# Kernel optimization log

Hardware: AMD Instinct MI355X
Metric: run time of the kernel (lower is better)

The kernel has to match this reference:

```python
import jax, jax.numpy as jnp
import numpy as np

N, F_IN, H, HEADS, C, E = 4096, 768, 512, 4, 32, 131072
DH = H // HEADS


def gcn_conv(x, W, b, src, dst):
    # PyG GCNConv: add self-loops, symmetric normalization, scatter-add aggregation
    h = x @ W                                   # [N, H_out]
    loop = jnp.arange(N)
    s = jnp.concatenate([src, loop])            # sources incl self-loops
    d = jnp.concatenate([dst, loop])            # targets incl self-loops
    deg = jax.ops.segment_sum(jnp.ones_like(d, dtype=h.dtype), d, num_segments=N)
    dinv = jnp.where(deg > 0, jax.lax.rsqrt(deg), 0.0)
    norm = dinv[s] * dinv[d]                    # [E+N]
    msg = h[s] * norm[:, None]                  # gather + scale
    out = jax.ops.segment_sum(msg, d, num_segments=N)  # scatter-add
    return out + b


def mha(x, in_w, in_b, out_w, out_b):
    # torch.nn.MultiheadAttention, batch=1, q=k=v=x, eval (no dropout)
    qkv = x @ in_w.T + in_b                     # [N, 3H]
    q, k, v = jnp.split(qkv, 3, axis=-1)
    q = q.reshape(N, HEADS, DH)
    k = k.reshape(N, HEADS, DH)
    v = v.reshape(N, HEADS, DH)
    scale = 1.0 / jnp.sqrt(jnp.asarray(DH, x.dtype))
    scores = jnp.einsum('nhd,mhd->hnm', q * scale, k)   # [HEADS, N, N]
    attn = jax.nn.softmax(scores, axis=-1)
    o = jnp.einsum('hnm,mhd->nhd', attn, v).reshape(N, H)
    return o @ out_w.T + out_b


def setup_inputs() -> dict:
    key = jax.random.key(0)
    ks = jax.random.split(key, 12)
    f32 = jnp.float32
    return {
        'x': jax.random.normal(ks[0], (N, F_IN), dtype=f32),
        'edge_index': jax.random.randint(ks[1], (2, E), 0, N, dtype=jnp.int64),
        'W1': jax.random.normal(ks[2], (F_IN, H), dtype=f32) * (1.0 / np.sqrt(F_IN)),
        'b1': jnp.zeros((H,), dtype=f32),
        'in_w': jax.random.normal(ks[3], (3 * H, H), dtype=f32) * (1.0 / np.sqrt(H)),
        'in_b': jnp.zeros((3 * H,), dtype=f32),
        'out_w': jax.random.normal(ks[4], (H, H), dtype=f32) * (1.0 / np.sqrt(H)),
        'out_b': jnp.zeros((H,), dtype=f32),
        'W2': jax.random.normal(ks[5], (H, H), dtype=f32) * (1.0 / np.sqrt(H)),
        'b2': jnp.zeros((H,), dtype=f32),
        'Wc': jax.random.normal(ks[6], (H, C), dtype=f32) * (1.0 / np.sqrt(H)),
        'bc': jnp.zeros((C,), dtype=f32),
    }


def reference(x, edge_index, W1, b1, in_w, in_b, out_w, out_b, W2, b2, Wc, bc):
    src, dst = edge_index[0], edge_index[1]
    h = jax.nn.relu(gcn_conv(x, W1, b1, src, dst))
    h = h + mha(h, in_w, in_b, out_w, out_b)      # residual; dropout is identity (eval)
    h = jax.nn.relu(gcn_conv(h, W2, b2, src, dst))
    return h @ Wc + bc                             # [N, C]
```

## Files before the change

kernel.cpp:

```cpp
#include <hip/hip_runtime.h>

typedef unsigned short u16;
typedef unsigned int u32;
typedef __attribute__((ext_vector_type(8))) short bf16x8;
typedef __attribute__((ext_vector_type(4))) short bf16x4;
typedef __attribute__((ext_vector_type(4))) float f32x4;
typedef __attribute__((ext_vector_type(16))) float f32x16;

__device__ __forceinline__ float b2f(u16 b){ u32 u = ((u32)b)<<16; float f; __builtin_memcpy(&f,&u,4); return f; }
__device__ __forceinline__ u16 f2b(float f){ u32 u; __builtin_memcpy(&u,&f,4); u32 r = (u + 0x7fffu + ((u>>16)&1u)) >> 16; return (u16)r; }
__device__ __forceinline__ u32 cvtpk(float lo, float hi){ u32 r; asm("v_cvt_pk_bf16_f32 %0, %1, %2" : "=v"(r) : "v"(lo), "v"(hi)); return r; }
__device__ __forceinline__ void pswap(u32 &a, u32 &b){ asm("v_permlane32_swap_b32 %0, %1" : "+v"(a), "+v"(b)); }

__global__ __launch_bounds__(256) void convert_bf16_k(const float* __restrict__ in, u16* __restrict__ out, int n){
  int i = (blockIdx.x*256 + threadIdx.x)*4;
  if (i + 3 < n){
    float4 v = *(const float4*)(in + i);
    bf16x4 o;
    o[0]=(short)f2b(v.x); o[1]=(short)f2b(v.y); o[2]=(short)f2b(v.z); o[3]=(short)f2b(v.w);
    *(bf16x4*)(out + i) = o;
  } else {
    for (; i<n; ++i) out[i]=f2b(in[i]);
  }
}

__global__ __launch_bounds__(256) void transpose_f32_bf16_k(const float* __restrict__ in, u16* __restrict__ out, int R, int C){
  __shared__ float tile[32][33];
  int tx = threadIdx.x & 31, ty = threadIdx.x >> 5;
  int c0 = blockIdx.x*32, r0 = blockIdx.y*32;
  #pragma unroll
  for (int k=0;k<4;++k){
    int r = r0 + ty + k*8, c = c0 + tx;
    if (r < R && c < C) tile[ty+k*8][tx] = in[(size_t)r*C + c];
  }
  __syncthreads();
  #pragma unroll
  for (int k=0;k<4;++k){
    int c = c0 + ty + k*8, r = r0 + tx;
    if (r < R && c < C) out[(size_t)c*R + r] = f2b(tile[tx][ty+k*8]);
  }
}

__global__ __launch_bounds__(256) void deg_init_k(int* __restrict__ deg, int n){
  int i = blockIdx.x*256 + threadIdx.x;
  if (i < n) deg[i] = 1;
}
__global__ __launch_bounds__(256) void deg_count_k(const int* __restrict__ dst, int* __restrict__ deg, int E){
  int e = blockIdx.x*256 + threadIdx.x;
  if (e < E) atomicAdd(&deg[dst[e]], 1);
}
__global__ __launch_bounds__(256) void scan_k(const int* __restrict__ deg, int* __restrict__ row_ptr,
                                              int* __restrict__ cursor, float* __restrict__ dinv){
  __shared__ int lds[256];
  int t = threadIdx.x;
  int base = t*16;
  int cnt[16]; int s = 0;
  #pragma unroll
  for (int k=0;k<16;++k){
    int d = deg[base+k];
    cnt[k] = d - 1;
    s += d - 1;
    dinv[base+k] = 1.0f / sqrtf((float)d);
  }
  lds[t] = s; __syncthreads();
  for (int o=1;o<256;o<<=1){
    int v = (t>=o) ? lds[t-o] : 0;
    __syncthreads();
    lds[t] += v;
    __syncthreads();
  }
  int run = lds[t] - s;
  #pragma unroll
  for (int k=0;k<16;++k){ row_ptr[base+k] = run; cursor[base+k] = run; run += cnt[k]; }
  if (t == 255) row_ptr[4096] = run;
}
__global__ __launch_bounds__(256) void scatter_k(const int* __restrict__ src, const int* __restrict__ dst,
                                                 int* __restrict__ cursor, int* __restrict__ srcl, int E){
  int e = blockIdx.x*256 + threadIdx.x;
  if (e < E){
    int d = dst[e];
    int pos = atomicAdd(&cursor[d], 1);
    srcl[pos] = src[e];
  }
}

__global__ __launch_bounds__(128) void aggregate_k(const u16* __restrict__ H, const float* __restrict__ dinv,
                                                   const int* __restrict__ rp, const int* __restrict__ srcl,
                                                   const float* __restrict__ bias, u16* __restrict__ out){
  const int i = blockIdx.x, t = threadIdx.x;
  const float di = dinv[i];
  bf16x4 hv = *(const bf16x4*)(H + (size_t)i*512 + t*4);
  float wself = di*di;
  float a0 = b2f((u16)hv[0])*wself, a1 = b2f((u16)hv[1])*wself, a2 = b2f((u16)hv[2])*wself, a3 = b2f((u16)hv[3])*wself;
  int e0 = rp[i], e1 = rp[i+1];
  for (int e=e0; e<e1; ++e){
    int s = srcl[e];
    float w = dinv[s]*di;
    bf16x4 v = *(const bf16x4*)(H + (size_t)s*512 + t*4);
    a0 += b2f((u16)v[0])*w; a1 += b2f((u16)v[1])*w; a2 += b2f((u16)v[2])*w; a3 += b2f((u16)v[3])*w;
  }
  a0 += bias[t*4+0]; a1 += bias[t*4+1]; a2 += bias[t*4+2]; a3 += bias[t*4+3];
  a0 = fmaxf(a0,0.f); a1 = fmaxf(a1,0.f); a2 = fmaxf(a2,0.f); a3 = fmaxf(a3,0.f);
  bf16x4 o; o[0]=(short)f2b(a0); o[1]=(short)f2b(a1); o[2]=(short)f2b(a2); o[3]=(short)f2b(a3);
  *(bf16x4*)(out + (size_t)i*512 + t*4) = o;
}

template<int BM,int BN,int WM,int WN,bool BIAS,bool RESID,bool RELU,bool OUTBF,bool QKV>
__global__ __launch_bounds__(256) void gemm_abt_k(
    const u16* __restrict__ A, const u16* __restrict__ B,
    const float* __restrict__ bias, const u16* __restrict__ resid,
    u16* __restrict__ vt, void* __restrict__ Cp, int M, int N, int K)
{
  constexpr int BK = 64;
  constexpr int AISS = (BM*BK)/(256*8);
  constexpr int BISS = (BN*BK)/(256*8);
  constexpr int WC = BN/WN;
  constexpr int FM = WM/16, FN = WN/16;
  constexpr float QS = 0.08838834764831845f;
  __shared__ u16 As[BM*BK];
  __shared__ u16 Bs[BN*BK];
  const int tid = threadIdx.x;
  const int wv = tid>>6, ln = tid&63;
  const int l15 = ln&15, l4 = ln>>4;
  const int wm = wv / WC, wn = wv % WC;
  const int bm0 = blockIdx.x*BM, bn0 = blockIdx.y*BN;
  const int arow = tid>>3;
  const int acol = (tid&7)*8;
  f32x4 acc[FM][FN];
  #pragma unroll
  for (int a=0;a<FM;++a)
    #pragma unroll
    for (int b=0;b<FN;++b) acc[a][b] = f32x4{0.f,0.f,0.f,0.f};
  bf16x8 ra[AISS], rb[BISS];
  #pragma unroll
  for (int i=0;i<AISS;++i) ra[i] = *(const bf16x8*)(A + (size_t)(bm0 + i*32 + arow)*K + acol);
  #pragma unroll
  for (int i=0;i<BISS;++i) rb[i] = *(const bf16x8*)(B + (size_t)(bn0 + i*32 + arow)*K + acol);
  for (int kt=0; kt<K; kt+=BK){
    #pragma unroll
    for (int i=0;i<AISS;++i) *(bf16x8*)(&As[i*2048 + tid*8]) = ra[i];
    #pragma unroll
    for (int i=0;i<BISS;++i) *(bf16x8*)(&Bs[i*2048 + tid*8]) = rb[i];
    __syncthreads();
    if (kt + BK < K){
      #pragma unroll
      for (int i=0;i<AISS;++i) ra[i] = *(const bf16x8*)(A + (size_t)(bm0 + i*32 + arow)*K + kt + BK + acol);
      #pragma unroll
      for (int i=0;i<BISS;++i) rb[i] = *(const bf16x8*)(B + (size_t)(bn0 + i*32 + arow)*K + kt + BK + acol);
    }
    #pragma unroll
    for (int kc=0;kc<2;++kc){
      bf16x8 af[FM], bfr[FN];
      #pragma unroll
      for (int a=0;a<FM;++a) af[a] = *(const bf16x8*)(&As[(wm*WM + a*16 + l15)*BK + kc*32 + l4*8]);
      #pragma unroll
      for (int b=0;b<FN;++b) bfr[b] = *(const bf16x8*)(&Bs[(wn*WN + b*16 + l15)*BK + kc*32 + l4*8]);
      #pragma unroll
      for (int a=0;a<FM;++a)
        #pragma unroll
        for (int b=0;b<FN;++b)
          acc[a][b] = __builtin_amdgcn_mfma_f32_16x16x32_bf16(af[a], bfr[b], acc[a][b], 0,0,0);
    }
    __syncthreads();
  }
  #pragma unroll
  for (int a=0;a<FM;++a)
    #pragma unroll
    for (int b=0;b<FN;++b){
      int r0 = bm0 + wm*WM + a*16 + l4*4;
      int c  = bn0 + wn*WN + b*16 + l15;
      if constexpr (QKV){
        float v0 = acc[a][b][0] + bias[c];
        float v1 = acc[a][b][1] + bias[c];
        float v2 = acc[a][b][2] + bias[c];
        float v3 = acc[a][b][3] + bias[c];
        if (c >= 1024){
          bf16x4 pk; pk[0]=(short)f2b(v0); pk[1]=(short)f2b(v1); pk[2]=(short)f2b(v2); pk[3]=(short)f2b(v3);
          *(bf16x4*)(vt + (size_t)(c-1024)*4096 + r0) = pk;
        } else {
          float s = (c < 512) ? QS : 1.0f;
          u16* o = (u16*)Cp;
          o[(size_t)(r0+0)*N + c] = f2b(v0*s);
          o[(size_t)(r0+1)*N + c] = f2b(v1*s);
          o[(size_t)(r0+2)*N + c] = f2b(v2*s);
          o[(size_t)(r0+3)*N + c] = f2b(v3*s);
        }
      } else {
        #pragma unroll
        for (int j=0;j<4;++j){
          int r = r0 + j;
          float v = acc[a][b][j];
          if (BIAS)  v += bias[c];
          if (RESID) v += b2f(resid[(size_t)r*N + c]);
          if (RELU)  v = fmaxf(v, 0.f);
          if (OUTBF) ((u16*)Cp)[(size_t)r*N + c] = f2b(v);
          else       ((float*)Cp)[(size_t)r*N + c] = v;
        }
      }
    }
}

__global__ __launch_bounds__(256,2) void attn_k(const u16* __restrict__ qkv, const u16* __restrict__ vtg,
                                                float* __restrict__ Op, float* __restrict__ Lp){
  __shared__ u16 Ks[64*128];
  __shared__ u16 Vs[128*128];
  const int head = blockIdx.y, split = blockIdx.z;
  const int qb0 = blockIdx.x*128;
  const int tid = threadIdx.x, wv = tid>>6, ln = tid&63;
  const int l31 = ln&31, hi = ln>>5;
  bf16x8 qf[8];
  {
    const u16* qp = qkv + (size_t)(qb0 + wv*32 + l31)*1536 + head*128 + hi*8;
    #pragma unroll
    for (int kk=0;kk<8;++kk) qf[kk] = *(const bf16x8*)(qp + kk*16);
  }
  f32x16 acc_o[4];
  #pragma unroll
  for (int d=0;d<4;++d)
    #pragma unroll
    for (int r=0;r<16;++r) acc_o[d][r] = 0.f;
  float l_part = 0.f;
  const int kR = ln, kG = wv*4;
  const int vR = tid>>1, vG = (tid&1)*4;
  const u16* kbase = qkv + 512 + (size_t)head*128;
  const u16* vbase = vtg + (size_t)(head*128 + vR)*4096;
  const int kv00 = split*1024;
  bf16x8 kreg[4], vreg[4];
  #pragma unroll
  for (int i=0;i<4;++i){
    kreg[i] = *(const bf16x8*)(kbase + (size_t)(kv00 + kR)*1536 + (kG+i)*8);
    vreg[i] = *(const bf16x8*)(vbase + kv00 + (vG+i)*8);
  }
  for (int it=0; it<16; ++it){
    #pragma unroll
    for (int i=0;i<4;++i){
      *(bf16x8*)((char*)Ks + kR*256 + (((kG+i)*16) ^ ((kR&15)<<4))) = kreg[i];
      *(bf16x8*)((char*)Vs + vR*256 + (((vG+i)*16) ^ ((vR&15)<<4))) = vreg[i];
    }
    __syncthreads();
    if (it < 15){
      int nb = kv00 + (it+1)*64;
      #pragma unroll
      for (int i=0;i<4;++i){
        kreg[i] = *(const bf16x8*)(kbase + (size_t)(nb + kR)*1536 + (kG+i)*8);
        vreg[i] = *(const bf16x8*)(vbase + nb + (vG+i)*8);
      }
    }
    f32x16 s0, s1;
    #pragma unroll
    for (int r=0;r<16;++r){ s0[r]=0.f; s1[r]=0.f; }
    #pragma unroll
    for (int kk=0;kk<8;++kk){
      int r0 = l31, r1 = 32 + l31;
      bf16x8 k0 = *(const bf16x8*)((char*)Ks + r0*256 + ((kk*32 + hi*16) ^ ((r0&15)<<4)));
      bf16x8 k1 = *(const bf16x8*)((char*)Ks + r1*256 + ((kk*32 + hi*16) ^ ((r1&15)<<4)));
      s0 = __builtin_amdgcn_mfma_f32_32x32x16_bf16(k0, qf[kk], s0, 0,0,0);
      s1 = __builtin_amdgcn_mfma_f32_32x32x16_bf16(k1, qf[kk], s1, 0,0,0);
    }
    union PU { u32 w[4]; bf16x8 v; };
    PU pa[4];
    #pragma unroll
    for (int g=0; g<2; ++g){
      float p[16];
      #pragma unroll
      for (int r=0;r<16;++r){ float sv = g ? s1[r] : s0[r]; p[r] = __expf(sv); l_part += p[r]; }
      u32 c0=cvtpk(p[0],p[1]), c1=cvtpk(p[2],p[3]), c2=cvtpk(p[4],p[5]), c3=cvtpk(p[6],p[7]);
      u32 c4=cvtpk(p[8],p[9]), c5=cvtpk(p[10],p[11]), c6=cvtpk(p[12],p[13]), c7=cvtpk(p[14],p[15]);
      pswap(c0,c2); pswap(c1,c3); pswap(c4,c6); pswap(c5,c7);
      pa[g*2+0].w[0]=c0; pa[g*2+0].w[1]=c1; pa[g*2+0].w[2]=c2; pa[g*2+0].w[3]=c3;
      pa[g*2+1].w[0]=c4; pa[g*2+1].w[1]=c5; pa[g*2+1].w[2]=c6; pa[g*2+1].w[3]=c7;
    }
    #pragma unroll
    for (int dg=0;dg<4;++dg){
      int row = dg*32 + l31;
      #pragma unroll
      for (int kvf=0;kvf<4;++kvf){
        bf16x8 vf = *(const bf16x8*)((char*)Vs + row*256 + ((kvf*32 + hi*16) ^ ((row&15)<<4)));
        acc_o[dg] = __builtin_amdgcn_mfma_f32_32x32x16_bf16(pa[kvf].v, vf, acc_o[dg], 0,0,0);
      }
    }
    __syncthreads();
  }
  float l_tot = l_part + __shfl_xor(l_part, 32, 64);
  if (hi == 0) Lp[split*4096 + qb0 + wv*32 + l31] = l_tot;
  #pragma unroll
  for (int dg=0;dg<4;++dg){
    #pragma unroll
    for (int r=0;r<16;++r){
      int q = qb0 + wv*32 + (r&3) + ((r>>2)<<3) + hi*4;
      Op[((size_t)split*4096 + q)*512 + head*128 + dg*32 + l31] = acc_o[dg][r];
    }
  }
}

__global__ __launch_bounds__(256) void combine_k(const float* __restrict__ Op, const float* __restrict__ Lp,
                                                 u16* __restrict__ oatt){
  int idx = blockIdx.x*256 + threadIdx.x;
  int n = idx >> 6, c8 = (idx & 63) << 3;
  float l = Lp[n] + Lp[4096+n] + Lp[8192+n] + Lp[12288+n];
  float inv = 1.0f/l;
  float acc[8] = {0,0,0,0,0,0,0,0};
  #pragma unroll
  for (int s=0;s<4;++s){
    const float* p = Op + ((size_t)(s*4096+n))*512 + c8;
    float4 u = *(const float4*)p;
    float4 v = *(const float4*)(p+4);
    acc[0]+=u.x; acc[1]+=u.y; acc[2]+=u.z; acc[3]+=u.w;
    acc[4]+=v.x; acc[5]+=v.y; acc[6]+=v.z; acc[7]+=v.w;
  }
  bf16x8 o;
  #pragma unroll
  for (int j=0;j<8;++j) o[j] = (short)f2b(acc[j]*inv);
  *(bf16x8*)(oatt + (size_t)n*512 + c8) = o;
}

extern "C" void kernel_launch(void* const* d_in, const int* in_sizes, int n_in,
                              void* d_out, int out_size, void* d_ws, size_t ws_size,
                              hipStream_t stream) {
  (void)n_in; (void)out_size; (void)ws_size;
  const float* x    = (const float*)d_in[0];
  const int*   ei   = (const int*)d_in[1];
  const float* W1   = (const float*)d_in[2];
  const float* b1   = (const float*)d_in[3];
  const float* inw  = (const float*)d_in[4];
  const float* inb  = (const float*)d_in[5];
  const float* outw = (const float*)d_in[6];
  const float* outb = (const float*)d_in[7];
  const float* W2   = (const float*)d_in[8];
  const float* b2   = (const float*)d_in[9];
  const float* Wc   = (const float*)d_in[10];
  const float* bc   = (const float*)d_in[11];
  float* out = (float*)d_out;
  const int E = in_sizes[1] / 2;
  const int* srcp = ei;
  const int* dstp = ei + E;

  char* base = (char*)d_ws;
  size_t off = 0;
  auto alloc = [&](size_t bytes)->void*{
    void* p = base + off;
    off = (off + bytes + 255) & ~((size_t)255);
    return p;
  };
  u16* Xb    = (u16*)alloc((size_t)4096*768*2);
  u16* W1T   = (u16*)alloc((size_t)512*768*2);
  u16* inWb  = (u16*)alloc((size_t)1536*512*2);
  u16* outWb = (u16*)alloc((size_t)512*512*2);
  u16* W2T   = (u16*)alloc((size_t)512*512*2);
  u16* WcT   = (u16*)alloc((size_t)32*512*2);
  u16* Hpre  = (u16*)alloc((size_t)4096*512*2);
  u16* h1    = (u16*)alloc((size_t)4096*512*2);
  u16* qkvb  = (u16*)alloc((size_t)4096*1536*2);
  u16* vtg   = (u16*)alloc((size_t)512*4096*2);
  u16* oatt  = (u16*)alloc((size_t)4096*512*2);
  u16* h2    = (u16*)alloc((size_t)4096*512*2);
  u16* h3    = (u16*)alloc((size_t)4096*512*2);
  float* Opart = (float*)alloc((size_t)4*4096*512*4);
  float* Lpart = (float*)alloc((size_t)4*4096*4);
  int*   deg  = (int*)alloc(4096*4);
  float* dinv = (float*)alloc(4096*4);
  int*   rowp = (int*)alloc(4097*4);
  int*   curs = (int*)alloc(4096*4);
  int*   srcl = (int*)alloc((size_t)E*4);

  convert_bf16_k<<<3072,256,0,stream>>>(x, Xb, 4096*768);
  convert_bf16_k<<<768,256,0,stream>>>(inw, inWb, 1536*512);
  convert_bf16_k<<<256,256,0,stream>>>(outw, outWb, 512*512);
  transpose_f32_bf16_k<<<dim3(16,24),256,0,stream>>>(W1, W1T, 768, 512);
  transpose_f32_bf16_k<<<dim3(16,16),256,0,stream>>>(W2, W2T, 512, 512);
  transpose_f32_bf16_k<<<dim3(1,16),256,0,stream>>>(Wc, WcT, 512, 32);

  deg_init_k<<<16,256,0,stream>>>(deg, 4096);
  deg_count_k<<<(E+255)/256,256,0,stream>>>(dstp, deg, E);
  scan_k<<<1,256,0,stream>>>(deg, rowp, curs, dinv);
  scatter_k<<<(E+255)/256,256,0,stream>>>(srcp, dstp, curs, srcl, E);

  gemm_abt_k<128,64,64,32,false,false,false,true,false><<<dim3(32,8),256,0,stream>>>(Xb, W1T, nullptr, nullptr, nullptr, Hpre, 4096, 512, 768);
  aggregate_k<<<4096,128,0,stream>>>(Hpre, dinv, rowp, srcl, b1, h1);

  gemm_abt_k<128,64,64,32,true,false,false,true,true><<<dim3(32,24),256,0,stream>>>(h1, inWb, inb, nullptr, vtg, qkvb, 4096, 1536, 512);
  attn_k<<<dim3(32,4,4),256,0,stream>>>(qkvb, vtg, Opart, Lpart);
  combine_k<<<1024,256,0,stream>>>(Opart, Lpart, oatt);
  gemm_abt_k<128,64,64,32,true,true,false,true,false><<<dim3(32,8),256,0,stream>>>(oatt, outWb, outb, h1, nullptr, h2, 4096, 512, 512);

  gemm_abt_k<128,64,64,32,false,false,false,true,false><<<dim3(32,8),256,0,stream>>>(h2, W2T, nullptr, nullptr, nullptr, Hpre, 4096, 512, 512);
  aggregate_k<<<4096,128,0,stream>>>(Hpre, dinv, rowp, srcl, b2, h3);

  gemm_abt_k<64,32,16,32,true,false,false,false,false><<<dim3(64,1),256,0,stream>>>(h3, WcT, bc, nullptr, nullptr, out, 4096, 32, 512);
}
```

Baseline: 186.0 us.

## Fuse prep kernels, use direct-to-LDS GEMM loads, split attention eight ways with bf16 partials

Merges the conversion, transpose and degree-count kernels into one launch, with the degree buffer zeroed by a memset. The GEMM now loads tiles through global_load_lds instead of register prefetch, which drops the software double-buffering. Attention splits the KV range eight ways with a smaller V tile and higher occupancy, folds log2(e) into the Q scale so it can use exp2, raises wave priority around the MFMA sections, and stores its partial outputs as bf16. The aim is fewer launches, more parallelism in attention and less partial-output traffic, at the cost of lost load/compute overlap in the GEMM and extra rounding in the partial sums.

```diff
diff --git a/kernel.cpp b/kernel.cpp
--- a/kernel.cpp
+++ b/kernel.cpp
@@ -11,9 +11,13 @@
 __device__ __forceinline__ u16 f2b(float f){ u32 u; __builtin_memcpy(&u,&f,4); u32 r = (u + 0x7fffu + ((u>>16)&1u)) >> 16; return (u16)r; }
 __device__ __forceinline__ u32 cvtpk(float lo, float hi){ u32 r; asm("v_cvt_pk_bf16_f32 %0, %1, %2" : "=v"(r) : "v"(lo), "v"(hi)); return r; }
 __device__ __forceinline__ void pswap(u32 &a, u32 &b){ asm("v_permlane32_swap_b32 %0, %1" : "+v"(a), "+v"(b)); }
-
-__global__ __launch_bounds__(256) void convert_bf16_k(const float* __restrict__ in, u16* __restrict__ out, int n){
-  int i = (blockIdx.x*256 + threadIdx.x)*4;
+__device__ __forceinline__ void gload16(const u16* g, u16* l){
+  __builtin_amdgcn_global_load_lds((const __attribute__((address_space(1))) void*)g,
+                                   (__attribute__((address_space(3))) void*)l, 16, 0, 0);
+}
+
+__device__ __forceinline__ void conv_body(const float* __restrict__ in, u16* __restrict__ out, int b, int n){
+  int i = (b*256 + threadIdx.x)*4;
   if (i + 3 < n){
     float4 v = *(const float4*)(in + i);
     bf16x4 o;
@@ -23,32 +27,40 @@
     for (; i<n; ++i) out[i]=f2b(in[i]);
   }
 }
-
-__global__ __launch_bounds__(256) void transpose_f32_bf16_k(const float* __restrict__ in, u16* __restrict__ out, int R, int C){
+__global__ __launch_bounds__(256) void prep_k(const float* __restrict__ x, const float* __restrict__ inw,
+    const float* __restrict__ outw, const float* __restrict__ W1, const float* __restrict__ W2,
+    const float* __restrict__ Wc, const int* __restrict__ dst, int E,
+    u16* __restrict__ Xb, u16* __restrict__ inWb, u16* __restrict__ outWb,
+    u16* __restrict__ W1T, u16* __restrict__ W2T, u16* __restrict__ WcT, int* __restrict__ deg){
   __shared__ float tile[32][33];
-  int tx = threadIdx.x & 31, ty = threadIdx.x >> 5;
-  int c0 = blockIdx.x*32, r0 = blockIdx.y*32;
-  #pragma unroll
-  for (int k=0;k<4;++k){
-    int r = r0 + ty + k*8, c = c0 + tx;
-    if (r < R && c < C) tile[ty+k*8][tx] = in[(size_t)r*C + c];
-  }
-  __syncthreads();
-  #pragma unroll
-  for (int k=0;k<4;++k){
-    int c = c0 + ty + k*8, r = r0 + tx;
-    if (r < R && c < C) out[(size_t)c*R + r] = f2b(tile[tx][ty+k*8]);
-  }
-}
-
-__global__ __launch_bounds__(256) void deg_init_k(int* __restrict__ deg, int n){
-  int i = blockIdx.x*256 + threadIdx.x;
-  if (i < n) deg[i] = 1;
-}
-__global__ __launch_bounds__(256) void deg_count_k(const int* __restrict__ dst, int* __restrict__ deg, int E){
-  int e = blockIdx.x*256 + threadIdx.x;
+  int b = blockIdx.x;
+  if (b < 3072){ conv_body(x, Xb, b, 4096*768); return; }
+  if (b < 3840){ conv_body(inw, inWb, b-3072, 1536*512); return; }
+  if (b < 4096){ conv_body(outw, outWb, b-3840, 512*512); return; }
+  if (b < 4752){
+    const float* in; u16* out; int R, C, bx, by;
+    if (b < 4480){ in=W1; out=W1T; R=768; C=512; int lb=b-4096; bx=lb&15; by=lb>>4; }
+    else if (b < 4736){ in=W2; out=W2T; R=512; C=512; int lb=b-4480; bx=lb&15; by=lb>>4; }
+    else { in=Wc; out=WcT; R=512; C=32; bx=0; by=b-4736; }
+    int tx = threadIdx.x & 31, ty = threadIdx.x >> 5;
+    int c0 = bx*32, r0 = by*32;
+    #pragma unroll
+    for (int k=0;k<4;++k){
+      int r = r0 + ty + k*8, c = c0 + tx;
+      if (r < R && c < C) tile[ty+k*8][tx] = in[(size_t)r*C + c];
+    }
+    __syncthreads();
+    #pragma unroll
+    for (int k=0;k<4;++k){
+      int c = c0 + ty + k*8, r = r0 + tx;
+      if (r < R && c < C) out[(size_t)c*R + r] = f2b(tile[tx][ty+k*8]);
+    }
+    return;
+  }
+  int e = (b-4752)*256 + threadIdx.x;
   if (e < E) atomicAdd(&deg[dst[e]], 1);
 }
+
 __global__ __launch_bounds__(256) void scan_k(const int* __restrict__ deg, int* __restrict__ row_ptr,
                                               int* __restrict__ cursor, float* __restrict__ dinv){
   __shared__ int lds[256];
@@ -57,7 +69,7 @@
   int cnt[16]; int s = 0;
   #pragma unroll
   for (int k=0;k<16;++k){
-    int d = deg[base+k];
+    int d = deg[base+k] + 1;
     cnt[k] = d - 1;
     s += d - 1;
     dinv[base+k] = 1.0f / sqrtf((float)d);
@@ -116,7 +128,7 @@
   constexpr int BISS = (BN*BK)/(256*8);
   constexpr int WC = BN/WN;
   constexpr int FM = WM/16, FN = WN/16;
-  constexpr float QS = 0.08838834764831845f;
+  constexpr float QS = 0.088388347648318447f * 1.4426950408889634f;
   __shared__ u16 As[BM*BK];
   __shared__ u16 Bs[BN*BK];
   const int tid = threadIdx.x;
@@ -131,23 +143,12 @@
   for (int a=0;a<FM;++a)
     #pragma unroll
     for (int b=0;b<FN;++b) acc[a][b] = f32x4{0.f,0.f,0.f,0.f};
-  bf16x8 ra[AISS], rb[BISS];
-  #pragma unroll
-  for (int i=0;i<AISS;++i) ra[i] = *(const bf16x8*)(A + (size_t)(bm0 + i*32 + arow)*K + acol);
-  #pragma unroll
-  for (int i=0;i<BISS;++i) rb[i] = *(const bf16x8*)(B + (size_t)(bn0 + i*32 + arow)*K + acol);
   for (int kt=0; kt<K; kt+=BK){
     #pragma unroll
-    for (int i=0;i<AISS;++i) *(bf16x8*)(&As[i*2048 + tid*8]) = ra[i];
-    #pragma unroll
-    for (int i=0;i<BISS;++i) *(bf16x8*)(&Bs[i*2048 + tid*8]) = rb[i];
-    __syncthreads();
-    if (kt + BK < K){
-      #pragma unroll
-      for (int i=0;i<AISS;++i) ra[i] = *(const bf16x8*)(A + (size_t)(bm0 + i*32 + arow)*K + kt + BK + acol);
-      #pragma unroll
-      for (int i=0;i<BISS;++i) rb[i] = *(const bf16x8*)(B + (size_t)(bn0 + i*32 + arow)*K + kt + BK + acol);
-    }
+    for (int i=0;i<AISS;++i) gload16(A + (size_t)(bm0 + i*32 + arow)*K + kt + acol, &As[i*2048 + wv*512]);
+    #pragma unroll
+    for (int i=0;i<BISS;++i) gload16(B + (size_t)(bn0 + i*32 + arow)*K + kt + acol, &Bs[i*2048 + wv*512]);
+    __syncthreads();
     #pragma unroll
     for (int kc=0;kc<2;++kc){
       bf16x8 af[FM], bfr[FN];
@@ -200,10 +201,10 @@
     }
 }
 
-__global__ __launch_bounds__(256,2) void attn_k(const u16* __restrict__ qkv, const u16* __restrict__ vtg,
-                                                float* __restrict__ Op, float* __restrict__ Lp){
+__global__ __launch_bounds__(256,4) void attn_k(const u16* __restrict__ qkv, const u16* __restrict__ vtg,
+                                                u16* __restrict__ Op, float* __restrict__ Lp){
   __shared__ u16 Ks[64*128];
-  __shared__ u16 Vs[128*128];
+  __shared__ u16 Vs[128*64];
   const int head = blockIdx.y, split = blockIdx.z;
   const int qb0 = blockIdx.x*128;
   const int tid = threadIdx.x, wv = tid>>6, ln = tid&63;
@@ -224,21 +225,21 @@
   const int vR = tid>>1, vG = (tid&1)*4;
   const u16* kbase = qkv + 512 + (size_t)head*128;
   const u16* vbase = vtg + (size_t)(head*128 + vR)*4096;
-  const int kv00 = split*1024;
+  const int kv00 = split*512;
   bf16x8 kreg[4], vreg[4];
   #pragma unroll
   for (int i=0;i<4;++i){
     kreg[i] = *(const bf16x8*)(kbase + (size_t)(kv00 + kR)*1536 + (kG+i)*8);
     vreg[i] = *(const bf16x8*)(vbase + kv00 + (vG+i)*8);
   }
-  for (int it=0; it<16; ++it){
+  for (int it=0; it<8; ++it){
     #pragma unroll
     for (int i=0;i<4;++i){
       *(bf16x8*)((char*)Ks + kR*256 + (((kG+i)*16) ^ ((kR&15)<<4))) = kreg[i];
-      *(bf16x8*)((char*)Vs + vR*256 + (((vG+i)*16) ^ ((vR&15)<<4))) = vreg[i];
-    }
-    __syncthreads();
-    if (it < 15){
+      *(bf16x8*)((char*)Vs + vR*128 + (((vG+i)*16) ^ ((vR&7)<<4))) = vreg[i];
+    }
+    __syncthreads();
+    if (it < 7){
       int nb = kv00 + (it+1)*64;
       #pragma unroll
       for (int i=0;i<4;++i){
@@ -249,6 +250,7 @@
     f32x16 s0, s1;
     #pragma unroll
     for (int r=0;r<16;++r){ s0[r]=0.f; s1[r]=0.f; }
+    __builtin_amdgcn_s_setprio(1);
     #pragma unroll
     for (int kk=0;kk<8;++kk){
       int r0 = l31, r1 = 32 + l31;
@@ -257,28 +259,31 @@
       s0 = __builtin_amdgcn_mfma_f32_32x32x16_bf16(k0, qf[kk], s0, 0,0,0);
       s1 = __builtin_amdgcn_mfma_f32_32x32x16_bf16(k1, qf[kk], s1, 0,0,0);
     }
+    __builtin_amdgcn_s_setprio(0);
     union PU { u32 w[4]; bf16x8 v; };
     PU pa[4];
     #pragma unroll
     for (int g=0; g<2; ++g){
       float p[16];
       #pragma unroll
-      for (int r=0;r<16;++r){ float sv = g ? s1[r] : s0[r]; p[r] = __expf(sv); l_part += p[r]; }
+      for (int r=0;r<16;++r){ float sv = g ? s1[r] : s0[r]; p[r] = __builtin_amdgcn_exp2f(sv); l_part += p[r]; }
       u32 c0=cvtpk(p[0],p[1]), c1=cvtpk(p[2],p[3]), c2=cvtpk(p[4],p[5]), c3=cvtpk(p[6],p[7]);
       u32 c4=cvtpk(p[8],p[9]), c5=cvtpk(p[10],p[11]), c6=cvtpk(p[12],p[13]), c7=cvtpk(p[14],p[15]);
       pswap(c0,c2); pswap(c1,c3); pswap(c4,c6); pswap(c5,c7);
       pa[g*2+0].w[0]=c0; pa[g*2+0].w[1]=c1; pa[g*2+0].w[2]=c2; pa[g*2+0].w[3]=c3;
       pa[g*2+1].w[0]=c4; pa[g*2+1].w[1]=c5; pa[g*2+1].w[2]=c6; pa[g*2+1].w[3]=c7;
     }
+    __builtin_amdgcn_s_setprio(1);
     #pragma unroll
     for (int dg=0;dg<4;++dg){
       int row = dg*32 + l31;
       #pragma unroll
       for (int kvf=0;kvf<4;++kvf){
-        bf16x8 vf = *(const bf16x8*)((char*)Vs + row*256 + ((kvf*32 + hi*16) ^ ((row&15)<<4)));
+        bf16x8 vf = *(const bf16x8*)((char*)Vs + row*128 + ((kvf*32 + hi*16) ^ ((row&7)<<4)));
         acc_o[dg] = __builtin_amdgcn_mfma_f32_32x32x16_bf16(pa[kvf].v, vf, acc_o[dg], 0,0,0);
       }
     }
+    __builtin_amdgcn_s_setprio(0);
     __syncthreads();
   }
   float l_tot = l_part + __shfl_xor(l_part, 32, 64);
@@ -288,25 +293,25 @@
     #pragma unroll
     for (int r=0;r<16;++r){
       int q = qb0 + wv*32 + (r&3) + ((r>>2)<<3) + hi*4;
-      Op[((size_t)split*4096 + q)*512 + head*128 + dg*32 + l31] = acc_o[dg][r];
-    }
-  }
-}
-
-__global__ __launch_bounds__(256) void combine_k(const float* __restrict__ Op, const float* __restrict__ Lp,
+      Op[((size_t)split*4096 + q)*512 + head*128 + dg*32 + l31] = f2b(acc_o[dg][r]);
+    }
+  }
+}
+
+__global__ __launch_bounds__(256) void combine_k(const u16* __restrict__ Op, const float* __restrict__ Lp,
                                                  u16* __restrict__ oatt){
   int idx = blockIdx.x*256 + threadIdx.x;
   int n = idx >> 6, c8 = (idx & 63) << 3;
-  float l = Lp[n] + Lp[4096+n] + Lp[8192+n] + Lp[12288+n];
+  float l = 0.f;
+  #pragma unroll
+  for (int s=0;s<8;++s) l += Lp[s*4096+n];
   float inv = 1.0f/l;
   float acc[8] = {0,0,0,0,0,0,0,0};
   #pragma unroll
-  for (int s=0;s<4;++s){
-    const float* p = Op + ((size_t)(s*4096+n))*512 + c8;
-    float4 u = *(const float4*)p;
-    float4 v = *(const float4*)(p+4);
-    acc[0]+=u.x; acc[1]+=u.y; acc[2]+=u.z; acc[3]+=u.w;
-    acc[4]+=v.x; acc[5]+=v.y; acc[6]+=v.z; acc[7]+=v.w;
+  for (int s=0;s<8;++s){
+    bf16x8 v = *(const bf16x8*)(Op + ((size_t)(s*4096+n))*512 + c8);
+    #pragma unroll
+    for (int j=0;j<8;++j) acc[j] += b2f((u16)v[j]);
   }
   bf16x8 o;
   #pragma unroll
@@ -355,23 +360,18 @@
   u16* oatt  = (u16*)alloc((size_t)4096*512*2);
   u16* h2    = (u16*)alloc((size_t)4096*512*2);
   u16* h3    = (u16*)alloc((size_t)4096*512*2);
-  float* Opart = (float*)alloc((size_t)4*4096*512*4);
-  float* Lpart = (float*)alloc((size_t)4*4096*4);
+  u16* Opart = (u16*)alloc((size_t)8*4096*512*2);
+  float* Lpart = (float*)alloc((size_t)8*4096*4);
   int*   deg  = (int*)alloc(4096*4);
   float* dinv = (float*)alloc(4096*4);
   int*   rowp = (int*)alloc(4097*4);
   int*   curs = (int*)alloc(4096*4);
   int*   srcl = (int*)alloc((size_t)E*4);
 
-  convert_bf16_k<<<3072,256,0,stream>>>(x, Xb, 4096*768);
-  convert_bf16_k<<<768,256,0,stream>>>(inw, inWb, 1536*512);
-  convert_bf16_k<<<256,256,0,stream>>>(outw, outWb, 512*512);
-  transpose_f32_bf16_k<<<dim3(16,24),256,0,stream>>>(W1, W1T, 768, 512);
-  transpose_f32_bf16_k<<<dim3(16,16),256,0,stream>>>(W2, W2T, 512, 512);
-  transpose_f32_bf16_k<<<dim3(1,16),256,0,stream>>>(Wc, WcT, 512, 32);
-
-  deg_init_k<<<16,256,0,stream>>>(deg, 4096);
-  deg_count_k<<<(E+255)/256,256,0,stream>>>(dstp, deg, E);
+  hipMemsetAsync(deg, 0, 4096*sizeof(int), stream);
+  int degBlocks = (E + 255)/256;
+  prep_k<<<4752 + degBlocks, 256, 0, stream>>>(x, inw, outw, W1, W2, Wc, dstp, E,
+                                               Xb, inWb, outWb, W1T, W2T, WcT, deg);
   scan_k<<<1,256,0,stream>>>(deg, rowp, curs, dinv);
   scatter_k<<<(E+255)/256,256,0,stream>>>(srcp, dstp, curs, srcl, E);
 
@@ -379,7 +379,7 @@
   aggregate_k<<<4096,128,0,stream>>>(Hpre, dinv, rowp, srcl, b1, h1);
 
   gemm_abt_k<128,64,64,32,true,false,false,true,true><<<dim3(32,24),256,0,stream>>>(h1, inWb, inb, nullptr, vtg, qkvb, 4096, 1536, 512);
-  attn_k<<<dim3(32,4,4),256,0,stream>>>(qkvb, vtg, Opart, Lpart);
+  attn_k<<<dim3(32,4,8),256,0,stream>>>(qkvb, vtg, Opart, Lpart);
   combine_k<<<1024,256,0,stream>>>(Opart, Lpart, oatt);
   gemm_abt_k<128,64,64,32,true,true,false,true,false><<<dim3(32,8),256,0,stream>>>(oatt, outWb, outb, h1, nullptr, h2, 4096, 512, 512);
 
```

Result: slower. 273.7 us (+47.2%).
